# Kernel tuning notes

Measured on AMD Instinct MI355X. Metric: run time of the kernel, lower is better.

## Reference

```python
import math
import jax, jax.numpy as jnp
import numpy as np

B, N, HID, NH = 4, 1024, 1024, 16
DH = HID // NH
MLP = int(HID * 4.0)


def _ndense(x, w):
    # NormalizedDense: row-normalize kernel (axis=1 for 2D), alpha=sqrt(w[0].size)=sqrt(out),
    # then divide by sqrt(fan_in).
    norm = jnp.linalg.norm(w, axis=1, keepdims=True)
    alpha = jnp.sqrt(jnp.asarray(w.shape[1], x.dtype))
    wn = w / (norm * alpha + 1e-4)
    wn = wn / jnp.sqrt(jnp.asarray(w.shape[0], x.dtype))
    return x @ wn


def mp_silu(x):
    return jax.nn.silu(x) / 0.596


def pixel_norm(x, eps=1e-4):
    return x * jax.lax.rsqrt(jnp.mean(x * x, axis=-1, keepdims=True) + eps)


def mp_add(a, b, t=0.3):
    return ((1 - t) * a + t * b) / math.sqrt((1 - t) ** 2 + t ** 2)


def setup_inputs() -> dict:
    key = jax.random.key(0)
    ks = jax.random.split(key, 9)
    std = 0.02
    return {
        "x": jax.random.normal(ks[0], (B, N, HID), jnp.float32),
        "c": jax.random.normal(ks[1], (B, HID), jnp.float32),
        "w_cond": std * jax.random.normal(ks[2], (HID, 2 * HID), jnp.float32),
        "w_qkv": std * jax.random.normal(ks[3], (HID, 3 * HID), jnp.float32),
        "w_out": std * jax.random.normal(ks[4], (HID, HID), jnp.float32),
        "w_mlp1": std * jax.random.normal(ks[5], (HID, MLP), jnp.float32),
        "w_mlp2": std * jax.random.normal(ks[6], (MLP, HID), jnp.float32),
        "attn_gain": 0.1 * jax.random.normal(ks[7], (), jnp.float32),
        "mlp_gain": 0.1 * jax.random.normal(ks[8], (), jnp.float32),
    }


def reference(x, c, w_cond, w_qkv, w_out, w_mlp1, w_mlp2, attn_gain, mlp_gain):
    # conditioning -> gain/shift
    cc = mp_silu(c)
    cc = _ndense(cc, w_cond)                       # [B, 2H]
    gain, shift = jnp.split(cc, 2, axis=-1)        # [B, H] each

    # attention branch
    x_cond = pixel_norm(x) * (1 + gain[:, None]) + shift[:, None]
    qkv = _ndense(x_cond, w_qkv)                   # [B, N, 3H]
    q, k, v = jnp.split(qkv, 3, axis=-1)
    q, k, v = pixel_norm(q), pixel_norm(k), pixel_norm(v)

    def split_heads(t):
        return t.reshape(B, N, NH, DH).transpose(0, 2, 1, 3)  # [B, NH, N, DH]

    q, k, v = split_heads(q), split_heads(k), split_heads(v)
    q = q / jnp.sqrt(jnp.sum(q * q, axis=-1, keepdims=True) + 1e-6)
    k = k / jnp.sqrt(jnp.sum(k * k, axis=-1, keepdims=True) + 1e-6)

    attn = jnp.einsum('bhnd,bhmd->bhnm', q, k) / math.sqrt(DH)
    attn = jax.nn.softmax(attn, axis=-1)
    x_attn = jnp.einsum('bhnm,bhmd->bhnd', attn, v)
    x_attn = x_attn.transpose(0, 2, 1, 3).reshape(B, N, HID)
    x_attn = pixel_norm(_ndense(x_attn, w_out)) * jnp.exp(attn_gain)
    x = mp_add(x, x_attn, t=0.3)

    # MLP branch
    x_cond = pixel_norm(x) * (1 + gain[:, None]) + shift[:, None]
    h = mp_silu(pixel_norm(_ndense(x_cond, w_mlp1)))
    x_mlp = pixel_norm(_ndense(h, w_mlp2)) * jnp.exp(mlp_gain)
    x = mp_add(x, x_mlp, t=0.3)
    return x
```

## Files before the change

### kernel.cpp

```cpp
#include <hip/hip_runtime.h>

typedef __bf16 bf16_t;
typedef __attribute__((ext_vector_type(8))) __bf16 bh8;
typedef __attribute__((ext_vector_type(4))) __bf16 bh4;
typedef __attribute__((ext_vector_type(4))) float f32x4;

#define DEV static __device__ __forceinline__

typedef __attribute__((address_space(3))) void lds_void;
typedef const __attribute__((address_space(1))) void glb_void;

DEV void async16(const bf16_t* g, bf16_t* l) {
  __builtin_amdgcn_global_load_lds((glb_void*)g, (lds_void*)l, 16, 0, 0);
}

DEV float wave_sum(float v) {
#pragma unroll
  for (int m = 32; m > 0; m >>= 1) v += __shfl_xor(v, m, 64);
  return v;
}

DEV float block_sum(float v, float* sbuf) {
  v = wave_sum(v);
  int wid = threadIdx.x >> 6;
  if ((threadIdx.x & 63) == 0) sbuf[wid] = v;
  __syncthreads();
  float r = sbuf[0] + sbuf[1] + sbuf[2] + sbuf[3];
  __syncthreads();
  return r;
}

__global__ void k_wnorm_all(const float* __restrict__ w_cond, const float* __restrict__ w_qkv,
                            const float* __restrict__ w_out, const float* __restrict__ w_mlp1,
                            const float* __restrict__ w_mlp2, float* __restrict__ s) {
  __shared__ float sbuf[4];
  int id = blockIdx.x;
  const float* W; int N, K, row;
  if (id < 1024)      { W = w_cond; N = 2048; K = 1024; row = id; }
  else if (id < 2048) { W = w_qkv;  N = 3072; K = 1024; row = id - 1024; }
  else if (id < 3072) { W = w_out;  N = 1024; K = 1024; row = id - 2048; }
  else if (id < 4096) { W = w_mlp1; N = 4096; K = 1024; row = id - 3072; }
  else                { W = w_mlp2; N = 1024; K = 4096; row = id - 4096; }
  const float4* wr = (const float4*)(W + (size_t)row * N);
  float acc = 0.f;
  for (int i = threadIdx.x; i < (N >> 2); i += 256) {
    float4 w = wr[i];
    acc += w.x*w.x + w.y*w.y + w.z*w.z + w.w*w.w;
  }
  float tot = block_sum(acc, sbuf);
  if (threadIdx.x == 0) {
    float norm = sqrtf(tot);
    s[id] = 1.0f / ((norm * sqrtf((float)N) + 1e-4f) * sqrtf((float)K));
  }
}

__global__ void k_wtrans_all(const float* __restrict__ w_cond, const float* __restrict__ w_qkv,
                             const float* __restrict__ w_out, const float* __restrict__ w_mlp1,
                             const float* __restrict__ w_mlp2, const float* __restrict__ sall,
                             bf16_t* __restrict__ wt_cond, bf16_t* __restrict__ wt_qkv,
                             bf16_t* __restrict__ wt_out, bf16_t* __restrict__ wt_mlp1,
                             bf16_t* __restrict__ wt_mlp2) {
  __shared__ float tile[64][65];
  int id = blockIdx.x;
  const float* W; const float* s; bf16_t* Wt; int K, N, n0, k0;
  if (id < 512)       { W=w_cond; s=sall;      Wt=wt_cond; K=1024; N=2048; int l=id;      n0=(l&31)*64; k0=(l>>5)*64; }
  else if (id < 1280) { W=w_qkv;  s=sall+1024; Wt=wt_qkv;  K=1024; N=3072; int l=id-512;  n0=(l%48)*64; k0=(l/48)*64; }
  else if (id < 1536) { W=w_out;  s=sall+2048; Wt=wt_out;  K=1024; N=1024; int l=id-1280; n0=(l&15)*64; k0=(l>>4)*64; }
  else if (id < 2560) { W=w_mlp1; s=sall+3072; Wt=wt_mlp1; K=1024; N=4096; int l=id-1536; n0=(l&63)*64; k0=(l>>6)*64; }
  else                { W=w_mlp2; s=sall+4096; Wt=wt_mlp2; K=4096; N=1024; int l=id-2560; n0=(l&15)*64; k0=(l>>4)*64; }
  int tx = threadIdx.x & 63, ty = threadIdx.x >> 6;
  for (int r = ty; r < 64; r += 4)
    tile[r][tx] = W[(size_t)(k0 + r) * N + n0 + tx] * s[k0 + r];
  __syncthreads();
  for (int r = ty; r < 64; r += 4)
    Wt[(size_t)(n0 + r) * K + k0 + tx] = (bf16_t)tile[tx][r];
}

__global__ void k_cond(const float* __restrict__ c, const bf16_t* __restrict__ wt,
                       float* __restrict__ gs) {
  __shared__ float cc[4][1024];
  int t = threadIdx.x;
  for (int i = t; i < 4096; i += 256) {
    int b = i >> 10, col = i & 1023;
    float x = c[b * 1024 + col];
    float sig = 1.f / (1.f + __expf(-x));
    cc[b][col] = x * sig * (1.f / 0.596f);
  }
  __syncthreads();
  int wid = t >> 6, lane = t & 63;
  int j = blockIdx.x * 4 + wid;
  const bf16_t* wr = wt + (size_t)j * 1024;
  float acc0 = 0, acc1 = 0, acc2 = 0, acc3 = 0;
  for (int i = lane; i < 1024; i += 64) {
    float w = (float)wr[i];
    acc0 += cc[0][i] * w; acc1 += cc[1][i] * w;
    acc2 += cc[2][i] * w; acc3 += cc[3][i] * w;
  }
  float v0 = wave_sum(acc0), v1 = wave_sum(acc1), v2 = wave_sum(acc2), v3 = wave_sum(acc3);
  if (lane == 0) {
    gs[0 * 2048 + j] = v0; gs[1 * 2048 + j] = v1;
    gs[2 * 2048 + j] = v2; gs[3 * 2048 + j] = v3;
  }
}

__global__ void k_xcond(const float* __restrict__ x, const float* __restrict__ gs,
                        bf16_t* __restrict__ xc) {
  __shared__ float sbuf[4];
  int row = blockIdx.x, b = row >> 10, t = threadIdx.x;
  float4 v = ((const float4*)(x + (size_t)row * 1024))[t];
  float ss = v.x*v.x + v.y*v.y + v.z*v.z + v.w*v.w;
  float tot = block_sum(ss, sbuf);
  float r = rsqrtf(tot * (1.f/1024.f) + 1e-4f);
  float4 g  = ((const float4*)(gs + b * 2048))[t];
  float4 sh = ((const float4*)(gs + b * 2048 + 1024))[t];
  bh4 o;
  o[0] = (bf16_t)(v.x * r * (1.f + g.x) + sh.x);
  o[1] = (bf16_t)(v.y * r * (1.f + g.y) + sh.y);
  o[2] = (bf16_t)(v.z * r * (1.f + g.z) + sh.z);
  o[3] = (bf16_t)(v.w * r * (1.f + g.w) + sh.w);
  *(bh4*)(xc + (size_t)row * 1024 + t * 4) = o;
}

__global__ __launch_bounds__(256) void k_gemm(const bf16_t* __restrict__ A,
                                              const bf16_t* __restrict__ Bt,
                                              bf16_t* __restrict__ C,
                                              int M, int N, int K, int klen) {
  __shared__ bf16_t As[2][128][32];
  __shared__ bf16_t Bs[2][128][32];
  const unsigned gx = gridDim.x;
  const unsigned flat = blockIdx.x + gx * blockIdx.y;
  const unsigned npx = gx >> 3;
  const unsigned xcd = flat & 7, o = flat >> 3;
  const unsigned grp = npx * 8;
  const unsigned mg = o / grp, rr = o % grp;
  const int m0 = (mg * 8 + rr / npx) * 128;
  const int n0 = (xcd * npx + rr % npx) * 128;
  const size_t kbeg = (size_t)blockIdx.z * klen;
  C += (size_t)blockIdx.z * M * N;
  const int t = threadIdx.x, lane = t & 63, wid = t >> 6;
  const int l15 = lane & 15, quad = lane >> 4;
  const int wm = (wid >> 1) * 64, wn = (wid & 1) * 64;
  const int r0 = t >> 2, kc0 = (t & 3) * 8;
  const bf16_t* Ag0 = A + (size_t)(m0 + r0) * K + kbeg + kc0;
  const bf16_t* Bg0 = Bt + (size_t)(n0 + r0) * K + kbeg + kc0;
  bf16_t* lA0 = &As[0][0][0] + wid * 512;
  bf16_t* lB0 = &Bs[0][0][0] + wid * 512;
  f32x4 acc[4][4] = {};
  for (int k0 = 0; k0 < klen; k0 += 64) {
#pragma unroll
    for (int h = 0; h < 2; h++) {
      async16(Ag0 + k0 + h * 32, lA0 + h * 4096);
      async16(Ag0 + k0 + h * 32 + (size_t)64 * K, lA0 + h * 4096 + 2048);
      async16(Bg0 + k0 + h * 32, lB0 + h * 4096);
      async16(Bg0 + k0 + h * 32 + (size_t)64 * K, lB0 + h * 4096 + 2048);
    }
    __syncthreads();
#pragma unroll
    for (int h = 0; h < 2; h++) {
      bh8 a[4], bb[4];
#pragma unroll
      for (int i = 0; i < 4; i++) a[i]  = *(const bh8*)&As[h][wm + i*16 + l15][quad*8];
#pragma unroll
      for (int j = 0; j < 4; j++) bb[j] = *(const bh8*)&Bs[h][wn + j*16 + l15][quad*8];
#pragma unroll
      for (int i = 0; i < 4; i++)
#pragma unroll
        for (int j = 0; j < 4; j++)
          acc[i][j] = __builtin_amdgcn_mfma_f32_16x16x32_bf16(a[i], bb[j], acc[i][j], 0, 0, 0);
    }
    __syncthreads();
  }
#pragma unroll
  for (int i = 0; i < 4; i++)
#pragma unroll
    for (int j = 0; j < 4; j++)
#pragma unroll
      for (int r2 = 0; r2 < 4; r2++)
        C[(size_t)(m0 + wm + i*16 + quad*4 + r2) * N + n0 + wn + j*16 + l15] =
            (bf16_t)acc[i][j][r2];
}

__global__ void k_qkvnorm(const bf16_t* __restrict__ qkv, bf16_t* __restrict__ qo,
                          bf16_t* __restrict__ ko, bf16_t* __restrict__ vo) {
  __shared__ float sbuf[4];
  const int row = blockIdx.x, b = row >> 10, n = row & 1023, t = threadIdx.x;
  const bf16_t* rp = qkv + (size_t)row * 3072;
  bh4 q4 = *(const bh4*)(rp + t * 4);
  bh4 k4 = *(const bh4*)(rp + 1024 + t * 4);
  bh4 v4 = *(const bh4*)(rp + 2048 + t * 4);
  float4 q = {(float)q4[0], (float)q4[1], (float)q4[2], (float)q4[3]};
  float4 k = {(float)k4[0], (float)k4[1], (float)k4[2], (float)k4[3]};
  float4 v = {(float)v4[0], (float)v4[1], (float)v4[2], (float)v4[3]};
  float sq = q.x*q.x + q.y*q.y + q.z*q.z + q.w*q.w;
  float sk = k.x*k.x + k.y*k.y + k.z*k.z + k.w*k.w;
  float sv = v.x*v.x + v.y*v.y + v.z*v.z + v.w*v.w;
  float tq = block_sum(sq, sbuf);
  float tk = block_sum(sk, sbuf);
  float tv = block_sum(sv, sbuf);
  float rq = rsqrtf(tq * (1.f/1024.f) + 1e-4f);
  float rk = rsqrtf(tk * (1.f/1024.f) + 1e-4f);
  float rv = rsqrtf(tv * (1.f/1024.f) + 1e-4f);
  float hq = sq, hk = sk;
#pragma unroll
  for (int m = 1; m < 16; m <<= 1) { hq += __shfl_xor(hq, m, 64); hk += __shfl_xor(hk, m, 64); }
  float qs = rq * rsqrtf(rq*rq*hq + 1e-6f);
  float ks = rk * rsqrtf(rk*rk*hk + 1e-6f);
  int h = t >> 4, d = (t & 15) * 4;
  size_t base = ((size_t)(b * 16 + h) * 1024 + n) * 64 + d;
  bh4 oq, okk, ov;
  oq[0]=(bf16_t)(q.x*qs); oq[1]=(bf16_t)(q.y*qs); oq[2]=(bf16_t)(q.z*qs); oq[3]=(bf16_t)(q.w*qs);
  okk[0]=(bf16_t)(k.x*ks); okk[1]=(bf16_t)(k.y*ks); okk[2]=(bf16_t)(k.z*ks); okk[3]=(bf16_t)(k.w*ks);
  ov[0]=(bf16_t)(v.x*rv); ov[1]=(bf16_t)(v.y*rv); ov[2]=(bf16_t)(v.z*rv); ov[3]=(bf16_t)(v.w*rv);
  *(bh4*)(qo + base) = oq;
  *(bh4*)(ko + base) = okk;
  *(bh4*)(vo + base) = ov;
}

__global__ void k_vtrans(const bf16_t* __restrict__ vh, bf16_t* __restrict__ vt) {
  __shared__ bf16_t tile[64][72];
  const int n0 = blockIdx.x * 64, bh = blockIdx.y;
  const int t = threadIdx.x;
  const bf16_t* src = vh + ((size_t)bh * 1024 + n0) * 64;
#pragma unroll
  for (int i = t; i < 512; i += 256) {
    int r = i >> 3, p = (i & 7) * 8;
    *(bh8*)&tile[r][p] = *(const bh8*)(src + r * 64 + p);
  }
  __syncthreads();
  bf16_t* dst = vt + (size_t)bh * 64 * 1024 + n0;
#pragma unroll
  for (int i = t; i < 512; i += 256) {
    int d = i & 63, nch = (i >> 6) * 8;
    bh8 o;
#pragma unroll
    for (int j = 0; j < 8; j++) o[j] = tile[nch + j][d];
    *(bh8*)(dst + (size_t)d * 1024 + nch) = o;
  }
}

__global__ __launch_bounds__(256) void k_attn(const bf16_t* __restrict__ Q,
                                              const bf16_t* __restrict__ K,
                                              const bf16_t* __restrict__ Vt_g,
                                              bf16_t* __restrict__ O) {
  __shared__ bf16_t Qs[64][72];
  __shared__ bf16_t Ks[64][72];
  __shared__ bf16_t Vt[64][72];
  __shared__ bf16_t Ps[64][72];
  const int qt = blockIdx.x, bh = blockIdx.y;
  const int b = bh >> 4, h = bh & 15;
  const int t = threadIdx.x, lane = t & 63, wid = t >> 6;
  const int l15 = lane & 15, quad = lane >> 4;
  const int strip = wid * 16;
  const bf16_t* Qg = Q + ((size_t)bh * 1024 + qt * 64) * 64;
  const bf16_t* Kg = K + (size_t)bh * 1024 * 64;
  const bf16_t* Vg = Vt_g + (size_t)bh * 64 * 1024;
  for (int i = t; i < 512; i += 256) {
    int r = i >> 3, p = (i & 7) * 8;
    *(bh8*)&Qs[r][p] = *(const bh8*)(Qg + r * 64 + p);
  }
  f32x4 o[4] = {};
  float rs[4] = {};
  __syncthreads();
  for (int kv0 = 0; kv0 < 1024; kv0 += 64) {
    for (int i = t; i < 512; i += 256) {
      int r = i >> 3, p = (i & 7) * 8;
      *(bh8*)&Ks[r][p] = *(const bh8*)(Kg + (size_t)(kv0 + r) * 64 + p);
      *(bh8*)&Vt[r][p] = *(const bh8*)(Vg + (size_t)r * 1024 + kv0 + p);
    }
    __syncthreads();
    f32x4 s[4] = {};
#pragma unroll
    for (int kc = 0; kc < 2; kc++) {
      bh8 aq = *(const bh8*)&Qs[strip + l15][kc*32 + quad*8];
      bh8 bk[4];
#pragma unroll
      for (int j = 0; j < 4; j++) bk[j] = *(const bh8*)&Ks[j*16 + l15][kc*32 + quad*8];
#pragma unroll
      for (int j = 0; j < 4; j++)
        s[j] = __builtin_amdgcn_mfma_f32_16x16x32_bf16(aq, bk[j], s[j], 0, 0, 0);
    }
#pragma unroll
    for (int j = 0; j < 4; j++)
#pragma unroll
      for (int r = 0; r < 4; r++) {
        float p = __expf(s[j][r] * 0.125f);
        bf16_t pb = (bf16_t)p;
        rs[r] += (float)pb;
        Ps[strip + quad*4 + r][j*16 + l15] = pb;
      }
#pragma unroll
    for (int kc = 0; kc < 2; kc++) {
      bh8 ap = *(const bh8*)&Ps[strip + l15][kc*32 + quad*8];
      bh8 bv[4];
#pragma unroll
      for (int j = 0; j < 4; j++) bv[j] = *(const bh8*)&Vt[j*16 + l15][kc*32 + quad*8];
#pragma unroll
      for (int j = 0; j < 4; j++)
        o[j] = __builtin_amdgcn_mfma_f32_16x16x32_bf16(ap, bv[j], o[j], 0, 0, 0);
    }
    __syncthreads();
  }
#pragma unroll
  for (int r = 0; r < 4; r++) {
    float v = rs[r];
    v += __shfl_xor(v, 1, 64); v += __shfl_xor(v, 2, 64);
    v += __shfl_xor(v, 4, 64); v += __shfl_xor(v, 8, 64);
    float inv = 1.f / v;
    int n = qt * 64 + strip + quad*4 + r;
#pragma unroll
    for (int j = 0; j < 4; j++)
      O[((size_t)b * 1024 + n) * 1024 + h*64 + j*16 + l15] = (bf16_t)(o[j][r] * inv);
  }
}

__global__ void k_amerge(const bf16_t* __restrict__ y, const float* __restrict__ x,
                         const float* __restrict__ gs, const float* __restrict__ again,
                         bf16_t* __restrict__ x1, bf16_t* __restrict__ xc2) {
  __shared__ float sbuf[4];
  int row = blockIdx.x, b = row >> 10, t = threadIdx.x;
  const size_t PS = (size_t)4096 * 1024;
  bh4 a0 = *(const bh4*)(y + (size_t)row * 1024 + t * 4);
  bh4 a1 = *(const bh4*)(y + PS + (size_t)row * 1024 + t * 4);
  float4 yv;
  yv.x = (float)a0[0] + (float)a1[0]; yv.y = (float)a0[1] + (float)a1[1];
  yv.z = (float)a0[2] + (float)a1[2]; yv.w = (float)a0[3] + (float)a1[3];
  float4 xv = ((const float4*)(x + (size_t)row * 1024))[t];
  float ss = yv.x*yv.x + yv.y*yv.y + yv.z*yv.z + yv.w*yv.w;
  float tot = block_sum(ss, sbuf);
  float r = rsqrtf(tot * (1.f/1024.f) + 1e-4f);
  float ag = __expf(again[0]);
  const float C1 = 0.7f / 0.76157731059f, C2 = 0.3f / 0.76157731059f;
  float4 xo;
  xo.x = C1 * xv.x + C2 * (yv.x * r * ag);
  xo.y = C1 * xv.y + C2 * (yv.y * r * ag);
  xo.z = C1 * xv.z + C2 * (yv.z * r * ag);
  xo.w = C1 * xv.w + C2 * (yv.w * r * ag);
  bh4 x1o;
  x1o[0] = (bf16_t)xo.x; x1o[1] = (bf16_t)xo.y; x1o[2] = (bf16_t)xo.z; x1o[3] = (bf16_t)xo.w;
  *(bh4*)(x1 + (size_t)row * 1024 + t * 4) = x1o;
  float ss1 = xo.x*xo.x + xo.y*xo.y + xo.z*xo.z + xo.w*xo.w;
  float tot1 = block_sum(ss1, sbuf);
  float r1 = rsqrtf(tot1 * (1.f/1024.f) + 1e-4f);
  float4 g  = ((const float4*)(gs + b * 2048))[t];
  float4 sh = ((const float4*)(gs + b * 2048 + 1024))[t];
  bh4 o;
  o[0] = (bf16_t)(xo.x * r1 * (1.f + g.x) + sh.x);
  o[1] = (bf16_t)(xo.y * r1 * (1.f + g.y) + sh.y);
  o[2] = (bf16_t)(xo.z * r1 * (1.f + g.z) + sh.z);
  o[3] = (bf16_t)(xo.w * r1 * (1.f + g.w) + sh.w);
  *(bh4*)(xc2 + (size_t)row * 1024 + t * 4) = o;
}

__global__ void k_mlpnorm(const bf16_t* __restrict__ hf, bf16_t* __restrict__ hb) {
  __shared__ float sbuf[4];
  int row = blockIdx.x, t = threadIdx.x;
  const bf16_t* rp = hf + (size_t)row * 4096;
  float4 v[4]; float ss = 0.f;
#pragma unroll
  for (int i = 0; i < 4; i++) {
    bh4 bv = *(const bh4*)(rp + (t + 256 * i) * 4);
    v[i].x = (float)bv[0]; v[i].y = (float)bv[1]; v[i].z = (float)bv[2]; v[i].w = (float)bv[3];
    ss += v[i].x*v[i].x + v[i].y*v[i].y + v[i].z*v[i].z + v[i].w*v[i].w;
  }
  float tot = block_sum(ss, sbuf);
  float r = rsqrtf(tot * (1.f/4096.f) + 1e-4f);
#pragma unroll
  for (int i = 0; i < 4; i++) {
    float a[4] = {v[i].x, v[i].y, v[i].z, v[i].w};
    bh4 o;
#pragma unroll
    for (int j = 0; j < 4; j++) {
      float u = a[j] * r;
      float sig = 1.f / (1.f + __expf(-u));
      o[j] = (bf16_t)(u * sig * (1.f / 0.596f));
    }
    *(bh4*)(hb + (size_t)row * 4096 + (t + 256 * i) * 4) = o;
  }
}

__global__ void k_fmerge(const bf16_t* __restrict__ y, const bf16_t* __restrict__ x1,
                         const float* __restrict__ mgain, float* __restrict__ out) {
  __shared__ float sbuf[4];
  int row = blockIdx.x, t = threadIdx.x;
  const size_t PS = (size_t)4096 * 1024;
  float4 yv = {0.f, 0.f, 0.f, 0.f};
#pragma unroll
  for (int p = 0; p < 2; p++) {
    bh4 yp = *(const bh4*)(y + p * PS + (size_t)row * 1024 + t * 4);
    yv.x += (float)yp[0]; yv.y += (float)yp[1]; yv.z += (float)yp[2]; yv.w += (float)yp[3];
  }
  bh4 xb = *(const bh4*)(x1 + (size_t)row * 1024 + t * 4);
  float4 xv = {(float)xb[0], (float)xb[1], (float)xb[2], (float)xb[3]};
  float ss = yv.x*yv.x + yv.y*yv.y + yv.z*yv.z + yv.w*yv.w;
  float tot = block_sum(ss, sbuf);
  float r = rsqrtf(tot * (1.f/1024.f) + 1e-4f);
  float mg = __expf(mgain[0]);
  const float C1 = 0.7f / 0.76157731059f, C2 = 0.3f / 0.76157731059f;
  float4 o;
  o.x = C1 * xv.x + C2 * (yv.x * r * mg);
  o.y = C1 * xv.y + C2 * (yv.y * r * mg);
  o.z = C1 * xv.z + C2 * (yv.z * r * mg);
  o.w = C1 * xv.w + C2 * (yv.w * r * mg);
  ((float4*)(out + (size_t)row * 1024))[t] = o;
}

extern "C" void kernel_launch(void* const* d_in, const int* in_sizes, int n_in,
                              void* d_out, int out_size, void* d_ws, size_t ws_size,
                              hipStream_t stream) {
  const float* x      = (const float*)d_in[0];
  const float* c      = (const float*)d_in[1];
  const float* w_cond = (const float*)d_in[2];
  const float* w_qkv  = (const float*)d_in[3];
  const float* w_out  = (const float*)d_in[4];
  const float* w_mlp1 = (const float*)d_in[5];
  const float* w_mlp2 = (const float*)d_in[6];
  const float* again  = (const float*)d_in[7];
  const float* mgain  = (const float*)d_in[8];
  float* out = (float*)d_out;
  char* ws = (char*)d_ws;

  bf16_t* wt_cond = (bf16_t*)(ws + 0);
  bf16_t* wt_qkv  = (bf16_t*)(ws + 4194304);
  bf16_t* wt_out  = (bf16_t*)(ws + 10485760);
  bf16_t* wt_mlp1 = (bf16_t*)(ws + 12582912);
  bf16_t* wt_mlp2 = (bf16_t*)(ws + 20971520);
  float*  sn      = (float*)(ws + 29360128);
  float*  gs      = (float*)(ws + 29392896);
  bf16_t* xc      = (bf16_t*)(ws + 29425664);
  bf16_t* qh      = (bf16_t*)(ws + 37814272);
  bf16_t* kh      = (bf16_t*)(ws + 46202880);
  bf16_t* vh      = (bf16_t*)(ws + 54591488);
  bf16_t* xattn   = (bf16_t*)(ws + 62980096);
  bf16_t* hb      = (bf16_t*)(ws + 37814272);
  bf16_t* x1      = (bf16_t*)(ws + 71368704);
  bf16_t* vt      = (bf16_t*)(ws + 79757312);
  bf16_t* buf_b   = (bf16_t*)(ws + 88145920);

  k_wnorm_all<<<8192, 256, 0, stream>>>(w_cond, w_qkv, w_out, w_mlp1, w_mlp2, sn);
  k_wtrans_all<<<3584, 256, 0, stream>>>(w_cond, w_qkv, w_out, w_mlp1, w_mlp2, sn,
                                         wt_cond, wt_qkv, wt_out, wt_mlp1, wt_mlp2);

  k_cond<<<512, 256, 0, stream>>>(c, wt_cond, gs);
  k_xcond<<<4096, 256, 0, stream>>>(x, gs, xc);
  k_gemm<<<dim3(24, 32, 1), 256, 0, stream>>>(xc, wt_qkv, buf_b, 4096, 3072, 1024, 1024);
  k_qkvnorm<<<4096, 256, 0, stream>>>(buf_b, qh, kh, vh);
  k_vtrans<<<dim3(16, 64), 256, 0, stream>>>(vh, vt);
  k_attn<<<dim3(16, 64), 256, 0, stream>>>(qh, kh, vt, xattn);
  k_gemm<<<dim3(8, 32, 2), 256, 0, stream>>>(xattn, wt_out, buf_b, 4096, 1024, 1024, 512);
  k_amerge<<<4096, 256, 0, stream>>>(buf_b, x, gs, again, x1, xc);
  k_gemm<<<dim3(32, 32, 1), 256, 0, stream>>>(xc, wt_mlp1, buf_b, 4096, 4096, 1024, 1024);
  k_mlpnorm<<<4096, 256, 0, stream>>>(buf_b, hb);
  k_gemm<<<dim3(8, 32, 2), 256, 0, stream>>>(hb, wt_mlp2, buf_b, 4096, 1024, 4096, 2048);
  k_fmerge<<<4096, 256, 0, stream>>>(buf_b, x1, mgain, out);
  (void)in_sizes; (void)n_in; (void)out_size; (void)ws_size;
}
```

Before: 387.3 us.

## Replace GEMM with 256x256-tile 8-wave kernel using interleaved prefetch pipeline

Replaces the 128x128, 4-wave GEMM with a 256x256-tile, 512-thread kernel. Each wave computes a 128x64 sub-tile, the LDS layout is swizzled, and async global-to-LDS loads of the next K tiles are interleaved between four MFMA phases. Those phases are separated by explicit barriers and raised wave priority. The split-K GEMMs move from 2 to 4 splits to keep enough workgroups, so the merge kernels now sum four partial buffers. The larger tiles cut global and LDS traffic per FLOP, but they bring more split-K partial traffic, higher register pressure, and fewer workgroups.

```diff
diff --git a/kernel.cpp b/kernel.cpp
--- a/kernel.cpp
+++ b/kernel.cpp
@@ -12,6 +12,13 @@
 
 DEV void async16(const bf16_t* g, bf16_t* l) {
   __builtin_amdgcn_global_load_lds((glb_void*)g, (lds_void*)l, 16, 0, 0);
+}
+
+#define GBAR() asm volatile("s_barrier" ::: "memory")
+#define VMW(n) asm volatile("s_waitcnt vmcnt(" #n ")" ::: "memory")
+
+DEV f32x4 mfma16(bh8 a, bh8 b, f32x4 c) {
+  return __builtin_amdgcn_mfma_f32_16x16x32_bf16(a, b, c, 0, 0, 0);
 }
 
 DEV float wave_sum(float v) {
@@ -121,63 +128,129 @@
   *(bh4*)(xc + (size_t)row * 1024 + t * 4) = o;
 }
 
-__global__ __launch_bounds__(256) void k_gemm(const bf16_t* __restrict__ A,
-                                              const bf16_t* __restrict__ Bt,
-                                              bf16_t* __restrict__ C,
-                                              int M, int N, int K, int klen) {
-  __shared__ bf16_t As[2][128][32];
-  __shared__ bf16_t Bs[2][128][32];
-  const unsigned gx = gridDim.x;
-  const unsigned flat = blockIdx.x + gx * blockIdx.y;
-  const unsigned npx = gx >> 3;
-  const unsigned xcd = flat & 7, o = flat >> 3;
-  const unsigned grp = npx * 8;
-  const unsigned mg = o / grp, rr = o % grp;
-  const int m0 = (mg * 8 + rr / npx) * 128;
-  const int n0 = (xcd * npx + rr % npx) * 128;
+__global__ __launch_bounds__(512, 2) void k_gemm8(const bf16_t* __restrict__ A,
+                                                  const bf16_t* __restrict__ Bt,
+                                                  bf16_t* __restrict__ C,
+                                                  int M, int N, int K, int klen) {
+  __shared__ __attribute__((aligned(16))) bf16_t As[2][2][256][32];
+  __shared__ __attribute__((aligned(16))) bf16_t Bs[2][2][256][32];
+  const int ntn = gridDim.x;
+  const unsigned flat = blockIdx.x + ntn * blockIdx.y;
+  const unsigned q = (ntn * gridDim.y) >> 3;
+  const unsigned wg = (flat & 7) * q + (flat >> 3);
+  const int m0 = (int)(wg / (unsigned)ntn) * 256;
+  const int n0 = (int)(wg % (unsigned)ntn) * 256;
   const size_t kbeg = (size_t)blockIdx.z * klen;
   C += (size_t)blockIdx.z * M * N;
-  const int t = threadIdx.x, lane = t & 63, wid = t >> 6;
+  const int t = threadIdx.x, lane = t & 63;
+  const int wm = (t >> 6) >> 2, wn = (t >> 6) & 3;
   const int l15 = lane & 15, quad = lane >> 4;
-  const int wm = (wid >> 1) * 64, wn = (wid & 1) * 64;
-  const int r0 = t >> 2, kc0 = (t & 3) * 8;
-  const bf16_t* Ag0 = A + (size_t)(m0 + r0) * K + kbeg + kc0;
-  const bf16_t* Bg0 = Bt + (size_t)(n0 + r0) * K + kbeg + kc0;
-  bf16_t* lA0 = &As[0][0][0] + wid * 512;
-  bf16_t* lB0 = &Bs[0][0][0] + wid * 512;
-  f32x4 acc[4][4] = {};
-  for (int k0 = 0; k0 < klen; k0 += 64) {
-#pragma unroll
-    for (int h = 0; h < 2; h++) {
-      async16(Ag0 + k0 + h * 32, lA0 + h * 4096);
-      async16(Ag0 + k0 + h * 32 + (size_t)64 * K, lA0 + h * 4096 + 2048);
-      async16(Bg0 + k0 + h * 32, lB0 + h * 4096);
-      async16(Bg0 + k0 + h * 32 + (size_t)64 * K, lB0 + h * 4096 + 2048);
-    }
-    __syncthreads();
-#pragma unroll
-    for (int h = 0; h < 2; h++) {
-      bh8 a[4], bb[4];
-#pragma unroll
-      for (int i = 0; i < 4; i++) a[i]  = *(const bh8*)&As[h][wm + i*16 + l15][quad*8];
-#pragma unroll
-      for (int j = 0; j < 4; j++) bb[j] = *(const bh8*)&Bs[h][wn + j*16 + l15][quad*8];
-#pragma unroll
-      for (int i = 0; i < 4; i++)
-#pragma unroll
-        for (int j = 0; j < 4; j++)
-          acc[i][j] = __builtin_amdgcn_mfma_f32_16x16x32_bf16(a[i], bb[j], acc[i][j], 0, 0, 0);
-    }
-    __syncthreads();
-  }
-#pragma unroll
-  for (int i = 0; i < 4; i++)
-#pragma unroll
-    for (int j = 0; j < 4; j++)
-#pragma unroll
-      for (int r2 = 0; r2 < 4; r2++)
-        C[(size_t)(m0 + wm + i*16 + quad*4 + r2) * N + n0 + wn + j*16 + l15] =
-            (bf16_t)acc[i][j][r2];
+  const int q8 = (quad ^ ((l15 >> 2) & 2)) * 8;
+  const int rA = wm * 128 + l15;
+  const int rB = wn * 64 + l15;
+  const int sr = t >> 2;
+  const int sc = ((t & 3) << 3) ^ ((t & 32) >> 1);
+  const int swv = (t >> 6) * 512;
+  const bf16_t* AgS = A + (size_t)(m0 + sr) * K + kbeg + sc;
+  const bf16_t* BgS = Bt + (size_t)(n0 + sr) * K + kbeg + sc;
+  const size_t rstep = (size_t)128 * K;
+  const int NT = klen >> 6;
+  f32x4 acc[8][4] = {};
+
+#define STG_A(kt_, h_, bb_) { const bf16_t* g = AgS + (kt_) * 64 + (h_) * 32; \
+    bf16_t* l = &As[bb_][h_][0][0] + swv; async16(g, l); async16(g + rstep, l + 4096); }
+#define STG_B(kt_, h_, bb_) { const bf16_t* g = BgS + (kt_) * 64 + (h_) * 32; \
+    bf16_t* l = &Bs[bb_][h_][0][0] + swv; async16(g, l); async16(g + rstep, l + 4096); }
+
+  STG_B(0, 0, 0); STG_B(0, 1, 0);
+  STG_A(0, 0, 0); STG_A(0, 1, 0);
+  if (NT > 1) { STG_B(1, 0, 1); STG_B(1, 1, 1); VMW(4); } else { VMW(0); }
+  GBAR();
+
+  for (int kt = 0; kt < NT; ++kt) {
+    const int bb = kt & 1;
+    bh8 a[4][2], b[4][2];
+#pragma unroll
+    for (int m = 0; m < 4; ++m)
+#pragma unroll
+      for (int kc = 0; kc < 2; ++kc)
+        a[m][kc] = *(const bh8*)&As[bb][kc][rA + m * 16][q8];
+#pragma unroll
+    for (int n = 0; n < 2; ++n)
+#pragma unroll
+      for (int kc = 0; kc < 2; ++kc)
+        b[n][kc] = *(const bh8*)&Bs[bb][kc][rB + n * 16][q8];
+    if (kt + 1 < NT) STG_A(kt + 1, 0, bb ^ 1);
+    GBAR();
+    __builtin_amdgcn_s_setprio(1);
+#pragma unroll
+    for (int m = 0; m < 4; ++m)
+#pragma unroll
+      for (int n = 0; n < 2; ++n)
+#pragma unroll
+        for (int kc = 0; kc < 2; ++kc)
+          acc[m][n] = mfma16(a[m][kc], b[n][kc], acc[m][n]);
+    __builtin_amdgcn_s_setprio(0);
+    GBAR();
+#pragma unroll
+    for (int n = 0; n < 2; ++n)
+#pragma unroll
+      for (int kc = 0; kc < 2; ++kc)
+        b[2 + n][kc] = *(const bh8*)&Bs[bb][kc][rB + (2 + n) * 16][q8];
+    if (kt + 1 < NT) STG_A(kt + 1, 1, bb ^ 1);
+    GBAR();
+    __builtin_amdgcn_s_setprio(1);
+#pragma unroll
+    for (int m = 0; m < 4; ++m)
+#pragma unroll
+      for (int n = 0; n < 2; ++n)
+#pragma unroll
+        for (int kc = 0; kc < 2; ++kc)
+          acc[m][2 + n] = mfma16(a[m][kc], b[2 + n][kc], acc[m][2 + n]);
+    __builtin_amdgcn_s_setprio(0);
+    GBAR();
+#pragma unroll
+    for (int m = 0; m < 4; ++m)
+#pragma unroll
+      for (int kc = 0; kc < 2; ++kc)
+        a[m][kc] = *(const bh8*)&As[bb][kc][rA + 64 + m * 16][q8];
+    if (kt + 2 < NT) STG_B(kt + 2, 0, bb);
+    GBAR();
+    __builtin_amdgcn_s_setprio(1);
+#pragma unroll
+    for (int m = 0; m < 4; ++m)
+#pragma unroll
+      for (int n = 0; n < 2; ++n)
+#pragma unroll
+        for (int kc = 0; kc < 2; ++kc)
+          acc[4 + m][n] = mfma16(a[m][kc], b[n][kc], acc[4 + m][n]);
+    __builtin_amdgcn_s_setprio(0);
+    GBAR();
+    if (kt + 2 < NT) STG_B(kt + 2, 1, bb);
+    __builtin_amdgcn_s_setprio(1);
+#pragma unroll
+    for (int m = 0; m < 4; ++m)
+#pragma unroll
+      for (int n = 0; n < 2; ++n)
+#pragma unroll
+        for (int kc = 0; kc < 2; ++kc)
+          acc[4 + m][2 + n] = mfma16(a[m][kc], b[2 + n][kc], acc[4 + m][2 + n]);
+    __builtin_amdgcn_s_setprio(0);
+    if (kt + 2 < NT) { VMW(4); } else { VMW(0); }
+    GBAR();
+  }
+#undef STG_A
+#undef STG_B
+
+  const int cm = m0 + wm * 128 + quad * 4;
+  const int cn = n0 + wn * 64 + l15;
+#pragma unroll
+  for (int m = 0; m < 8; ++m)
+#pragma unroll
+    for (int n = 0; n < 4; ++n)
+#pragma unroll
+      for (int r2 = 0; r2 < 4; ++r2)
+        C[(size_t)(cm + m * 16 + r2) * N + cn + n * 16] = (bf16_t)acc[m][n][r2];
 }
 
 __global__ void k_qkvnorm(const bf16_t* __restrict__ qkv, bf16_t* __restrict__ qo,
@@ -319,11 +392,12 @@
   __shared__ float sbuf[4];
   int row = blockIdx.x, b = row >> 10, t = threadIdx.x;
   const size_t PS = (size_t)4096 * 1024;
-  bh4 a0 = *(const bh4*)(y + (size_t)row * 1024 + t * 4);
-  bh4 a1 = *(const bh4*)(y + PS + (size_t)row * 1024 + t * 4);
-  float4 yv;
-  yv.x = (float)a0[0] + (float)a1[0]; yv.y = (float)a0[1] + (float)a1[1];
-  yv.z = (float)a0[2] + (float)a1[2]; yv.w = (float)a0[3] + (float)a1[3];
+  float4 yv = {0.f, 0.f, 0.f, 0.f};
+#pragma unroll
+  for (int p = 0; p < 4; p++) {
+    bh4 a = *(const bh4*)(y + p * PS + (size_t)row * 1024 + t * 4);
+    yv.x += (float)a[0]; yv.y += (float)a[1]; yv.z += (float)a[2]; yv.w += (float)a[3];
+  }
   float4 xv = ((const float4*)(x + (size_t)row * 1024))[t];
   float ss = yv.x*yv.x + yv.y*yv.y + yv.z*yv.z + yv.w*yv.w;
   float tot = block_sum(ss, sbuf);
@@ -385,7 +459,7 @@
   const size_t PS = (size_t)4096 * 1024;
   float4 yv = {0.f, 0.f, 0.f, 0.f};
 #pragma unroll
-  for (int p = 0; p < 2; p++) {
+  for (int p = 0; p < 4; p++) {
     bh4 yp = *(const bh4*)(y + p * PS + (size_t)row * 1024 + t * 4);
     yv.x += (float)yp[0]; yv.y += (float)yp[1]; yv.z += (float)yp[2]; yv.w += (float)yp[3];
   }
@@ -442,15 +516,15 @@
 
   k_cond<<<512, 256, 0, stream>>>(c, wt_cond, gs);
   k_xcond<<<4096, 256, 0, stream>>>(x, gs, xc);
-  k_gemm<<<dim3(24, 32, 1), 256, 0, stream>>>(xc, wt_qkv, buf_b, 4096, 3072, 1024, 1024);
+  k_gemm8<<<dim3(12, 16, 1), 512, 0, stream>>>(xc, wt_qkv, buf_b, 4096, 3072, 1024, 1024);
   k_qkvnorm<<<4096, 256, 0, stream>>>(buf_b, qh, kh, vh);
   k_vtrans<<<dim3(16, 64), 256, 0, stream>>>(vh, vt);
   k_attn<<<dim3(16, 64), 256, 0, stream>>>(qh, kh, vt, xattn);
-  k_gemm<<<dim3(8, 32, 2), 256, 0, stream>>>(xattn, wt_out, buf_b, 4096, 1024, 1024, 512);
+  k_gemm8<<<dim3(4, 16, 4), 512, 0, stream>>>(xattn, wt_out, buf_b, 4096, 1024, 1024, 256);
   k_amerge<<<4096, 256, 0, stream>>>(buf_b, x, gs, again, x1, xc);
-  k_gemm<<<dim3(32, 32, 1), 256, 0, stream>>>(xc, wt_mlp1, buf_b, 4096, 4096, 1024, 1024);
+  k_gemm8<<<dim3(16, 16, 1), 512, 0, stream>>>(xc, wt_mlp1, buf_b, 4096, 4096, 1024, 1024);
   k_mlpnorm<<<4096, 256, 0, stream>>>(buf_b, hb);
-  k_gemm<<<dim3(8, 32, 2), 256, 0, stream>>>(hb, wt_mlp2, buf_b, 4096, 1024, 4096, 2048);
+  k_gemm8<<<dim3(4, 16, 4), 512, 0, stream>>>(hb, wt_mlp2, buf_b, 4096, 1024, 4096, 1024);
   k_fmerge<<<4096, 256, 0, stream>>>(buf_b, x1, mgain, out);
   (void)in_sizes; (void)n_in; (void)out_size; (void)ws_size;
 }
```

Result: faster. 368.9 us (-4.8%).
